# Performance work log

Measured on AMD Instinct MI355X. Metric: run time of the kernel, lower is better.

Reference implementation:

```python
import jax, jax.numpy as jnp
import numpy as np

B, T, D, H, L, K = 64, 512, 256, 256, 2, 3


def setup_inputs() -> dict:
    key = jax.random.key(0)
    ks = jax.random.split(key, 12)
    s = 0.05
    f = jnp.float32
    return {
        "x": jax.random.normal(ks[0], (B, T, D), f),
        # GRUCell params per layer (torch gate order: r, z, n)
        "W_ih": jax.random.normal(ks[1], (L, 3 * H, H), f) * s,
        "b_ih": jax.random.normal(ks[2], (L, 3 * H), f) * s,
        "W_hh": jax.random.normal(ks[3], (L, 3 * H, H), f) * s,
        "b_hh": jax.random.normal(ks[4], (L, 3 * H), f) * s,
        # refinement cell params per layer
        "Wg": jax.random.normal(ks[5], (L, H, 2 * H), f) * s,
        "bg": jax.random.normal(ks[6], (L, H), f) * s,
        "Wt": jax.random.normal(ks[7], (L, H, 2 * H), f) * s,
        "bt": jax.random.normal(ks[8], (L, H), f) * s,
        "Wu": jax.random.normal(ks[9], (L, H, H), f) * s,
        "bu": jax.random.normal(ks[10], (L, H), f) * s,
    }


def reference(x, W_ih, b_ih, W_hh, b_hh, Wg, bg, Wt, bt, Wu, bu):
    def step(hidden, x_t):  # hidden: (L, B, H), x_t: (B, D)
        inp = x_t
        new_hiddens = []
        for l in range(L):
            h = hidden[l]
            # GRU cell (torch semantics)
            gi = inp @ W_ih[l].T + b_ih[l]
            gh = h @ W_hh[l].T + b_hh[l]
            i_r, i_z, i_n = jnp.split(gi, 3, axis=-1)
            h_r, h_z, h_n = jnp.split(gh, 3, axis=-1)
            r = jax.nn.sigmoid(i_r + h_r)
            z = jax.nn.sigmoid(i_z + h_z)
            n = jnp.tanh(i_n + r * h_n)
            h_new = (1.0 - z) * n + z * h
            # recursive refinement
            out = h_new
            rh = h_new
            for _ in range(K):
                comb = jnp.concatenate([out, rh], axis=-1)  # (B, 2H)
                g = jax.nn.sigmoid(comb @ Wg[l].T + bg[l])
                ref = jnp.tanh(comb @ Wt[l].T + bt[l])
                out = g * ref + (1.0 - g) * out
                rh = jnp.tanh(out @ Wu[l].T + bu[l])
            new_hiddens.append(h_new)
            inp = out
        return jnp.stack(new_hiddens, axis=0), inp

    hidden0 = jnp.zeros((L, B, H), x.dtype)
    final_hidden, outs = jax.lax.scan(step, hidden0, jnp.swapaxes(x, 0, 1))
    output = jnp.swapaxes(outs, 0, 1)  # (B, T, H)
    return output, final_hidden
```

## Files before the change

kernel.cpp:

```cpp
#include <hip/hip_runtime.h>

typedef float  f32x4  __attribute__((ext_vector_type(4)));
typedef __bf16 bf16x8 __attribute__((ext_vector_type(8)));

#define NB 64
#define NT 512
#define ND 256
#define NH 256
#define NROW (NB*NT)

#define OFF_WIH 0
#define OFF_WHH 393216
#define OFF_WGT 786432
#define OFF_WU  1310720
#define W_TOTAL 1441792
#define OFF_GI   (W_TOTAL)
#define OFF_OUT0 (OFF_GI + 512*64*768)
#define OFF_OUT1 (OFF_OUT0 + NROW*256)
#define OFF_FLAG (OFF_OUT1 + NROW*256)

#define NW 128

__device__ inline unsigned short f2bu(float f){
  unsigned int u = __builtin_bit_cast(unsigned int, f);
  unsigned int r = u + 0x7fffu + ((u >> 16) & 1u);
  return (unsigned short)(r >> 16);
}
__device__ inline float bf2f(unsigned short u){
  unsigned int v = ((unsigned int)u) << 16;
  return __builtin_bit_cast(float, v);
}
__device__ inline float sigm(float x){ return 1.0f / (1.0f + __expf(-x)); }
__device__ inline float tanhf_(float x){ return 1.0f - 2.0f / (__expf(2.0f * x) + 1.0f); }

#define MFMA(a,b,c) __builtin_amdgcn_mfma_f32_16x16x32_bf16((a),(b),(c),0,0,0)

__device__ inline void gload_lds16(const void* g, void* l){
  __builtin_amdgcn_global_load_lds(
    (const __attribute__((address_space(1))) unsigned int*)g,
    (__attribute__((address_space(3))) unsigned int*)l, 16, 0, 0);
}
__device__ inline bf16x8 ldG(const unsigned short* p){
  return *reinterpret_cast<const bf16x8*>(p);
}
template<int SLP>
__device__ inline void spin_ge(int* p, int tgt){
  while (__hip_atomic_load(p, __ATOMIC_RELAXED, __HIP_MEMORY_SCOPE_AGENT) < tgt)
    __builtin_amdgcn_s_sleep(SLP);
}

__global__ void cvt_weights(const float* __restrict__ Wih, const float* __restrict__ Whh,
                            const float* __restrict__ Wg,  const float* __restrict__ Wt,
                            const float* __restrict__ Wu,  unsigned short* __restrict__ ws){
  int i = blockIdx.x * blockDim.x + threadIdx.x;
  if (i < OFF_WHH) {
    ws[i] = f2bu(Wih[i]);
  } else if (i < OFF_WGT) {
    ws[i] = f2bu(Whh[i - OFF_WHH]);
  } else if (i < OFF_WU) {
    int j = i - OFF_WGT;
    int l = j >> 18; int r = (j >> 9) & 511; int k = j & 511;
    float v = (r < 256) ? Wg[(l * 256 + r) * 512 + k]
                        : Wt[(l * 256 + (r - 256)) * 512 + k];
    ws[i] = f2bu(v);
  } else if (i < W_TOTAL) {
    ws[i] = f2bu(Wu[i - OFF_WU]);
  }
}

__global__ void pack_x(const float* __restrict__ x, unsigned short* __restrict__ xin){
  size_t i = ((size_t)blockIdx.x * blockDim.x + threadIdx.x) * 4;
  float4 v = *reinterpret_cast<const float4*>(x + i);
  ushort4 u; u.x = f2bu(v.x); u.y = f2bu(v.y); u.z = f2bu(v.z); u.w = f2bu(v.w);
  *reinterpret_cast<ushort4*>(xin + i) = u;
}

__global__ __launch_bounds__(1024) void gi_gemm(
    const unsigned short* __restrict__ xin,
    const unsigned short* __restrict__ wih,
    const float* __restrict__ bih, const float* __restrict__ bhh,
    unsigned short* __restrict__ gi)
{
  __shared__ alignas(16) unsigned short sA[64 * 256];
  const int tid = threadIdx.x, blk = blockIdx.x;
  const int ln = tid & 63, wv = tid >> 6, m = ln & 15, lg = ln >> 4;
  {
    const char* src = (const char*)(xin + (size_t)blk * 64 * 256);
    #pragma unroll
    for (int i = 0; i < 2; ++i){
      int o = tid * 16 + i * 16384;
      int r = o >> 9, wb = o & 511;
      gload_lds16(src + (size_t)r * 512 + (wb ^ ((r & 7) << 4)), (char*)sA + o);
    }
  }
  __syncthreads();
  f32x4 acc[3][4] = {};
  #pragma unroll
  for (int kc = 0; kc < 8; ++kc){
    int kk = kc * 32 + lg * 8;
    bf16x8 a[4];
    #pragma unroll
    for (int mt = 0; mt < 4; ++mt){
      int row = mt * 16 + m;
      a[mt] = *(const bf16x8*)((const char*)sA + row * 512 + ((kk * 2) ^ ((row & 7) << 4)));
    }
    #pragma unroll
    for (int g = 0; g < 3; ++g){
      bf16x8 b = ldG(wih + (size_t)(g * 256 + wv * 16 + m) * 256 + kk);
      #pragma unroll
      for (int mt = 0; mt < 4; ++mt) acc[g][mt] = MFMA(a[mt], b, acc[g][mt]);
    }
  }
  const int c = wv * 16 + m;
  #pragma unroll
  for (int g = 0; g < 3; ++g){
    float bias = bih[g * 256 + c] + (g < 2 ? bhh[g * 256 + c] : 0.f);
    #pragma unroll
    for (int mt = 0; mt < 4; ++mt){
      #pragma unroll
      for (int j = 0; j < 4; ++j){
        int row = blk * 64 + mt * 16 + lg * 4 + j;
        int b = row >> 9, t = row & 511;
        gi[((size_t)t * 64 + b) * 768 + g * 256 + c] = f2bu(acc[g][mt][j] + bias);
      }
    }
  }
}

__device__ void chain_role(
    int grp, const unsigned short* __restrict__ gi, const unsigned short* __restrict__ whh,
    const float* __restrict__ bhh, unsigned short* __restrict__ outw,
    float* __restrict__ hfin, int* prog, int* bd, char* smem)
{
  __builtin_amdgcn_s_setprio(1);
  char* hAc = smem;
  const int tid = threadIdx.x;
  const int ln  = tid & 63, wv = tid >> 6;
  const int m   = ln & 15;
  const int lg  = ln >> 4;

  f32x4 wf[3][2][8];
  #pragma unroll
  for (int g = 0; g < 3; ++g)
    #pragma unroll
    for (int s = 0; s < 2; ++s){
      const unsigned short* p = whh + (size_t)(g * 256 + wv * 32 + s * 16 + m) * 256;
      #pragma unroll
      for (int kc = 0; kc < 8; ++kc){
        wf[g][s][kc] = *reinterpret_cast<const f32x4*>(p + kc * 32 + lg * 8);
        asm volatile("" : "+v"(wf[g][s][kc]));
      }
    }

  const int bb   = lg & 1;
  const int su   = lg >> 1;
  const int wcol = wv * 32 + su * 16 + m;
  const int brow = grp * 2 + bb;
  const float bNv = bhh[512 + wcol];

  const int arow  = m & 1;
  const int arows = arow << 4;
  const int rbase = arow * 512;
  const int wbyte = bb * 512 + ((wcol * 2) ^ (bb << 4));

  const unsigned short* gbase = gi + (size_t)brow * 768 + wcol;
  unsigned short* op = outw + (size_t)brow * NT * 256 + wcol;

  if (tid < 256){
    ((unsigned int*)hAc)[tid] = 0;
    ((unsigned int*)(hAc + 1024))[tid] = 0;
  }
  if (bd){
    if (tid == 0){ spin_ge<8>(&bd[0], 16); spin_ge<8>(&bd[1], 16); __threadfence(); }
    __syncthreads();
    (void)__hip_atomic_load(&bd[0], __ATOMIC_ACQUIRE, __HIP_MEMORY_SCOPE_AGENT);
  }
  unsigned int gAr = gbase[0], gAz = gbase[256], gAn = gbase[512];
  unsigned int gBr = gbase[49152], gBz = gbase[49152 + 256], gBn = gbase[49152 + 512];
  float h = 0.f;
  __syncthreads();

  auto body = [&](int t, int curo, unsigned int& GR, unsigned int& GZ, unsigned int& GN){
    float xr = bf2f((unsigned short)GR);
    float xz = bf2f((unsigned short)GZ);
    float xn = bf2f((unsigned short)GN);
    if (t + 2 < NT){
      const unsigned short* gp = gbase + (size_t)(t + 2) * 49152;
      GR = gp[0]; GZ = gp[256]; GN = gp[512];
    }
    f32x4 a00{}, a01{}, a10{}, a11{}, a20{}, a21{};
    #pragma unroll
    for (int kc = 0; kc < 8; ++kc){
      int kb = kc * 64 + lg * 16;
      bf16x8 hv = *(const bf16x8*)(hAc + curo + rbase + (kb ^ arows));
      a00 = MFMA(hv, __builtin_bit_cast(bf16x8, wf[0][0][kc]), a00);
      a01 = MFMA(hv, __builtin_bit_cast(bf16x8, wf[0][1][kc]), a01);
      a10 = MFMA(hv, __builtin_bit_cast(bf16x8, wf[1][0][kc]), a10);
      a11 = MFMA(hv, __builtin_bit_cast(bf16x8, wf[1][1][kc]), a11);
      a20 = MFMA(hv, __builtin_bit_cast(bf16x8, wf[2][0][kc]), a20);
      a21 = MFMA(hv, __builtin_bit_cast(bf16x8, wf[2][1][kc]), a21);
    }
    float aR = su ? (bb ? a01[1] : a01[0]) : (bb ? a00[1] : a00[0]);
    float aZ = su ? (bb ? a11[1] : a11[0]) : (bb ? a10[1] : a10[0]);
    float aN = su ? (bb ? a21[1] : a21[0]) : (bb ? a20[1] : a20[0]);
    float R = sigm(aR + xr);
    float Z = sigm(aZ + xz);
    float N = tanhf_(xn + R * (aN + bNv));
    h = N + Z * (h - N);
    unsigned short hb = f2bu(h);
    *(unsigned short*)(hAc + (curo ^ 1024) + wbyte) = hb;
    op[t * 256] = hb;
    asm volatile("s_waitcnt lgkmcnt(0)" ::: "memory");
    __builtin_amdgcn_sched_barrier(0);
    __builtin_amdgcn_s_barrier();
    __builtin_amdgcn_sched_barrier(0);
  };

  for (int tp = 0; tp < NT; tp += 2){
    if ((tp & 15) == 0){
      if (tp > 0){
        __syncthreads();
        if (tid == 0){
          __threadfence();
          __hip_atomic_store(prog, tp, __ATOMIC_RELEASE, __HIP_MEMORY_SCOPE_AGENT);
        }
      }
      if (bd){
        int B1 = (tp >> 4) + 1;
        if (B1 < 32){
          if (tid == 0){ spin_ge<8>(&bd[B1], 16); __threadfence(); }
          __syncthreads();
          (void)__hip_atomic_load(&bd[B1], __ATOMIC_ACQUIRE, __HIP_MEMORY_SCOPE_AGENT);
        }
      }
    }
    body(tp,     0,    gAr, gAz, gAn);
    body(tp + 1, 1024, gBr, gBz, gBn);
  }
  __syncthreads();
  if (tid == 0){
    __threadfence();
    __hip_atomic_store(prog, NT, __ATOMIC_RELEASE, __HIP_MEMORY_SCOPE_AGENT);
  }
  hfin[(size_t)brow * 256 + wcol] = h;
}

__device__ void worker_role(
    int w, unsigned short* __restrict__ gi,
    const unsigned short* __restrict__ outw0, const unsigned short* __restrict__ outw1,
    const unsigned short* __restrict__ wsb,
    const float* __restrict__ bih, const float* __restrict__ bhh,
    const float* __restrict__ bg, const float* __restrict__ bt, const float* __restrict__ bu,
    float* __restrict__ o, int* flags, char* smem)
{
  const int tid = threadIdx.x;
  const int ln = tid & 63, wv = tid >> 6, m = ln & 15, lg = ln >> 4;

  auto ldA = [&](int row, int kbyte) -> bf16x8 {
    return *(const bf16x8*)(smem + row * 1024 + (kbyte ^ ((row & 7) << 4)));
  };

  for (int i = w; i < 1024; i += NW){
    const int lay = i >> 9, t = i & 511;
    int* prog = &flags[lay * 32];
    if (tid == 0){
      for (int q = 0; q < 32; ++q) spin_ge<32>(&prog[q], t + 1);
      __threadfence();
    }
    __syncthreads();
    (void)__hip_atomic_load(&prog[0], __ATOMIC_ACQUIRE, __HIP_MEMORY_SCOPE_AGENT);

    const unsigned short* src0 = lay ? outw1 : outw0;
    #pragma unroll
    for (int q = 0; q < 8; ++q){
      int ofs = tid * 16 + q * 8192;
      int r = ofs >> 10, wb = ofs & 1023;
      int wb2 = (wb ^ ((r & 7) << 4)) & 511;
      gload_lds16((const char*)(src0 + ((size_t)r * NT + t) * 256) + wb2, smem + ofs);
    }
    __syncthreads();

    const unsigned short* wgt = wsb + OFF_WGT + (size_t)lay * 512 * 512;
    const unsigned short* wu  = wsb + OFF_WU  + (size_t)lay * 256 * 256;
    const float* bgp = bg + lay * 256;
    const float* btp = bt + lay * 256;
    const float* bup = bu + lay * 256;

    for (int iter = 0; iter < 3; ++iter){
      float oo0[4][4], oo1[4][4];
      {
        f32x4 ag[4] = {}, at4[4] = {};
        #pragma unroll 2
        for (int kc = 0; kc < 16; ++kc){
          int kk = kc * 32 + lg * 8;
          bf16x8 Bg = ldG(wgt + (size_t)(      wv * 32 + m) * 512 + kk);
          bf16x8 Bt = ldG(wgt + (size_t)(256 + wv * 32 + m) * 512 + kk);
          #pragma unroll
          for (int mt = 0; mt < 4; ++mt){
            bf16x8 A = ldA(mt * 16 + m, kk * 2);
            ag[mt]  = MFMA(A, Bg, ag[mt]);
            at4[mt] = MFMA(A, Bt, at4[mt]);
          }
        }
        int col = wv * 32 + m;
        float bgv = bgp[col], btv = btp[col];
        #pragma unroll
        for (int mt = 0; mt < 4; ++mt)
          #pragma unroll
          for (int j = 0; j < 4; ++j){
            int row = mt * 16 + lg * 4 + j;
            float old = bf2f(*(unsigned short*)(smem + row * 1024 + ((col * 2) ^ ((row & 7) << 4))));
            float g  = sigm(ag[mt][j] + bgv);
            float rf = tanhf_(at4[mt][j] + btv);
            oo0[mt][j] = g * rf + (1.f - g) * old;
          }
      }
      {
        f32x4 ag[4] = {}, at4[4] = {};
        #pragma unroll 2
        for (int kc = 0; kc < 16; ++kc){
          int kk = kc * 32 + lg * 8;
          bf16x8 Bg = ldG(wgt + (size_t)(      wv * 32 + 16 + m) * 512 + kk);
          bf16x8 Bt = ldG(wgt + (size_t)(256 + wv * 32 + 16 + m) * 512 + kk);
          #pragma unroll
          for (int mt = 0; mt < 4; ++mt){
            bf16x8 A = ldA(mt * 16 + m, kk * 2);
            ag[mt]  = MFMA(A, Bg, ag[mt]);
            at4[mt] = MFMA(A, Bt, at4[mt]);
          }
        }
        int col = wv * 32 + 16 + m;
        float bgv = bgp[col], btv = btp[col];
        #pragma unroll
        for (int mt = 0; mt < 4; ++mt)
          #pragma unroll
          for (int j = 0; j < 4; ++j){
            int row = mt * 16 + lg * 4 + j;
            float old = bf2f(*(unsigned short*)(smem + row * 1024 + ((col * 2) ^ ((row & 7) << 4))));
            float g  = sigm(ag[mt][j] + bgv);
            float rf = tanhf_(at4[mt][j] + btv);
            oo1[mt][j] = g * rf + (1.f - g) * old;
          }
      }
      __syncthreads();
      if (iter == 2 && lay == 1){
        #pragma unroll
        for (int mt = 0; mt < 4; ++mt)
          #pragma unroll
          for (int j = 0; j < 4; ++j){
            int b = mt * 16 + lg * 4 + j;
            o[((size_t)b * NT + t) * 256 + wv * 32 + m]      = oo0[mt][j];
            o[((size_t)b * NT + t) * 256 + wv * 32 + 16 + m] = oo1[mt][j];
          }
      } else {
        #pragma unroll
        for (int mt = 0; mt < 4; ++mt)
          #pragma unroll
          for (int j = 0; j < 4; ++j){
            int row = mt * 16 + lg * 4 + j;
            int c0 = wv * 32 + m, c1 = wv * 32 + 16 + m;
            *(unsigned short*)(smem + row * 1024 + ((c0 * 2) ^ ((row & 7) << 4))) = f2bu(oo0[mt][j]);
            *(unsigned short*)(smem + row * 1024 + ((c1 * 2) ^ ((row & 7) << 4))) = f2bu(oo1[mt][j]);
          }
        __syncthreads();
        if (iter < 2){
          #pragma unroll
          for (int s = 0; s < 2; ++s){
            f32x4 au[4] = {};
            #pragma unroll
            for (int kc = 0; kc < 8; ++kc){
              int kk = kc * 32 + lg * 8;
              bf16x8 Bu = ldG(wu + (size_t)(wv * 32 + s * 16 + m) * 256 + kk);
              #pragma unroll
              for (int mt = 0; mt < 4; ++mt)
                au[mt] = MFMA(ldA(mt * 16 + m, kk * 2), Bu, au[mt]);
            }
            int col = wv * 32 + s * 16 + m;
            float buv = bup[col];
            #pragma unroll
            for (int mt = 0; mt < 4; ++mt)
              #pragma unroll
              for (int j = 0; j < 4; ++j){
                int row = mt * 16 + lg * 4 + j;
                *(unsigned short*)(smem + row * 1024 + (((512 + col * 2)) ^ ((row & 7) << 4)))
                    = f2bu(tanhf_(au[mt][j] + buv));
              }
          }
          __syncthreads();
        }
      }
    }
    if (lay == 0){
      const unsigned short* wih1 = wsb + OFF_WIH + (size_t)768 * 256;
      #pragma unroll
      for (int q = 0; q < 6; ++q){
        int tile = wv + 8 * q;
        int cg = tile * 16 + m;
        f32x4 acc[4] = {};
        #pragma unroll
        for (int kc = 0; kc < 8; ++kc){
          int kk = kc * 32 + lg * 8;
          bf16x8 B = ldG(wih1 + (size_t)cg * 256 + kk);
          #pragma unroll
          for (int mt = 0; mt < 4; ++mt)
            acc[mt] = MFMA(ldA(mt * 16 + m, kk * 2), B, acc[mt]);
        }
        float bias = bih[768 + cg] + (cg < 512 ? bhh[768 + cg] : 0.f);
        #pragma unroll
        for (int mt = 0; mt < 4; ++mt)
          #pragma unroll
          for (int j = 0; j < 4; ++j){
            int b = mt * 16 + lg * 4 + j;
            gi[((size_t)t * 64 + b) * 768 + cg] = f2bu(acc[mt][j] + bias);
          }
      }
      __syncthreads();
      if (tid == 0){
        __threadfence();
        __hip_atomic_fetch_add(&flags[64 + (t >> 4)], 1, __ATOMIC_RELEASE, __HIP_MEMORY_SCOPE_AGENT);
      }
    } else {
      __syncthreads();
    }
  }
}

__global__ __launch_bounds__(512, 2) void mega(
    unsigned short* __restrict__ gi, const unsigned short* __restrict__ wsb,
    const float* __restrict__ bih, const float* __restrict__ bhh,
    const float* __restrict__ bg, const float* __restrict__ bt, const float* __restrict__ bu,
    unsigned short* __restrict__ outw0, unsigned short* __restrict__ outw1,
    float* __restrict__ o, float* __restrict__ hf, int* flags)
{
  extern __shared__ char smem[];
  const int role = blockIdx.x;
  if (role < NW){
    worker_role(role, gi, outw0, outw1, wsb, bih, bhh, bg, bt, bu, o, flags, smem);
  } else if (role < NW + 32){
    chain_role(role - NW, gi, wsb + OFF_WHH, bhh, outw0, hf,
               &flags[role - NW], nullptr, smem);
  } else {
    chain_role(role - NW - 32, gi, wsb + OFF_WHH + 768 * 256, bhh + 768, outw1,
               hf + 64 * 256, &flags[32 + (role - NW - 32)], &flags[64], smem);
  }
}

extern "C" void kernel_launch(void* const* d_in, const int* in_sizes, int n_in,
                              void* d_out, int out_size, void* d_ws, size_t ws_size,
                              hipStream_t stream) {
  const float* x   = (const float*)d_in[0];
  const float* Wih = (const float*)d_in[1];
  const float* bih = (const float*)d_in[2];
  const float* Whh = (const float*)d_in[3];
  const float* bhh = (const float*)d_in[4];
  const float* Wg  = (const float*)d_in[5];
  const float* bg  = (const float*)d_in[6];
  const float* Wt  = (const float*)d_in[7];
  const float* bt  = (const float*)d_in[8];
  const float* Wu  = (const float*)d_in[9];
  const float* bu  = (const float*)d_in[10];
  unsigned short* ws = (unsigned short*)d_ws;
  float* o  = (float*)d_out;
  float* hf = o + (size_t)NB * NT * NH;

  unsigned short* gi    = ws + OFF_GI;
  unsigned short* outw0 = ws + OFF_OUT0;
  unsigned short* outw1 = ws + OFF_OUT1;
  unsigned short* xin   = ws + OFF_OUT1;
  int* flags = (int*)(ws + OFF_FLAG);

  const int MEGA_LDS = 100 * 1024;
  (void)hipFuncSetAttribute((const void*)mega,
                            hipFuncAttributeMaxDynamicSharedMemorySize, MEGA_LDS);

  cvt_weights<<<W_TOTAL / 256, 256, 0, stream>>>(Wih, Whh, Wg, Wt, Wu, ws);
  pack_x<<<(NROW * 256 / 4) / 256, 256, 0, stream>>>(x, xin);
  gi_gemm<<<512, 1024, 0, stream>>>(xin, ws + OFF_WIH, bih, bhh, gi);
  (void)hipMemsetAsync(flags, 0, 96 * sizeof(int), stream);
  mega<<<NW + 64, 512, MEGA_LDS, stream>>>(gi, ws, bih, bhh, bg, bt, bu,
                                           outw0, outw1, o, hf, flags);
}
```

Measured before the change: 1.085 ms.

## Stage GI blocks into LDS in chain role and dynamically schedule layer-1 refinement

The recurrent chain blocks now copy each 16-timestep block of precomputed input-gate values into a double-buffered LDS area with async loads, instead of issuing scattered per-step global loads. Layer-1 refinement tasks are no longer statically assigned to worker blocks; any block that finishes its role, chain blocks included, pulls timesteps from an atomic job counter. The goal is to take global-load latency off the serial recurrence and to use chain blocks for the layer-1 tail work. The cost is more LDS use and counter contention, and chain blocks now exit early into the work queue.

```diff
diff --git a/kernel.cpp b/kernel.cpp
--- a/kernel.cpp
+++ b/kernel.cpp
@@ -76,8 +76,7 @@
 }
 
 __global__ __launch_bounds__(1024) void gi_gemm(
-    const unsigned short* __restrict__ xin,
-    const unsigned short* __restrict__ wih,
+    const unsigned short* __restrict__ xin, const unsigned short* __restrict__ wih,
     const float* __restrict__ bih, const float* __restrict__ bhh,
     unsigned short* __restrict__ gi)
 {
@@ -133,7 +132,8 @@
     float* __restrict__ hfin, int* prog, int* bd, char* smem)
 {
   __builtin_amdgcn_s_setprio(1);
-  char* hAc = smem;
+  char* sGI = smem;
+  char* hAc = smem + 98304;
   const int tid = threadIdx.x;
   const int ln  = tid & 63, wv = tid >> 6;
   const int m   = ln & 15;
@@ -162,32 +162,47 @@
   const int arows = arow << 4;
   const int rbase = arow * 512;
   const int wbyte = bb * 512 + ((wcol * 2) ^ (bb << 4));
-
-  const unsigned short* gbase = gi + (size_t)brow * 768 + wcol;
+  const int goff  = bb * 1536 + wcol * 2;
+
+  const char* gsrc = (const char*)gi + (size_t)(grp * 2) * 1536;
   unsigned short* op = outw + (size_t)brow * NT * 256 + wcol;
 
   if (tid < 256){
     ((unsigned int*)hAc)[tid] = 0;
     ((unsigned int*)(hAc + 1024))[tid] = 0;
   }
-  if (bd){
-    if (tid == 0){ spin_ge<8>(&bd[0], 16); spin_ge<8>(&bd[1], 16); __threadfence(); }
-    __syncthreads();
-    (void)__hip_atomic_load(&bd[0], __ATOMIC_ACQUIRE, __HIP_MEMORY_SCOPE_AGENT);
-  }
-  unsigned int gAr = gbase[0], gAz = gbase[256], gAn = gbase[512];
-  unsigned int gBr = gbase[49152], gBz = gbase[49152 + 256], gBn = gbase[49152 + 512];
+
+  auto bdwait = [&](int B){
+    if (bd && B < 32){
+      if (tid == 0){ spin_ge<8>(&bd[B], 16); __threadfence(); }
+      __syncthreads();
+      (void)__hip_atomic_load(&bd[B], __ATOMIC_ACQUIRE, __HIP_MEMORY_SCOPE_AGENT);
+    }
+  };
+  auto stage = [&](int B){
+    char* dst = sGI + (B & 1) * 49152;
+    const char* src = gsrc + (size_t)B * 16 * 98304;
+    #pragma unroll
+    for (int r = 0; r < 6; ++r){
+      int o = tid * 16 + r * 8192;
+      int tl = o / 3072;
+      int wi = o - tl * 3072;
+      gload_lds16(src + (size_t)tl * 98304 + wi, dst + o);
+    }
+  };
+
+  bdwait(0);
+  stage(0);
+  asm volatile("s_waitcnt vmcnt(0)" ::: "memory");
+  __syncthreads();
+
   float h = 0.f;
-  __syncthreads();
-
-  auto body = [&](int t, int curo, unsigned int& GR, unsigned int& GZ, unsigned int& GN){
-    float xr = bf2f((unsigned short)GR);
-    float xz = bf2f((unsigned short)GZ);
-    float xn = bf2f((unsigned short)GN);
-    if (t + 2 < NT){
-      const unsigned short* gp = gbase + (size_t)(t + 2) * 49152;
-      GR = gp[0]; GZ = gp[256]; GN = gp[512];
-    }
+
+  auto body = [&](int t, int curo){
+    const char* gp = sGI + ((t >> 4) & 1) * 49152 + (t & 15) * 3072 + goff;
+    unsigned short ur = *(const unsigned short*)(gp);
+    unsigned short uz = *(const unsigned short*)(gp + 512);
+    unsigned short un = *(const unsigned short*)(gp + 1024);
     f32x4 a00{}, a01{}, a10{}, a11{}, a20{}, a21{};
     #pragma unroll
     for (int kc = 0; kc < 8; ++kc){
@@ -203,9 +218,9 @@
     float aR = su ? (bb ? a01[1] : a01[0]) : (bb ? a00[1] : a00[0]);
     float aZ = su ? (bb ? a11[1] : a11[0]) : (bb ? a10[1] : a10[0]);
     float aN = su ? (bb ? a21[1] : a21[0]) : (bb ? a20[1] : a20[0]);
-    float R = sigm(aR + xr);
-    float Z = sigm(aZ + xz);
-    float N = tanhf_(xn + R * (aN + bNv));
+    float R = sigm(aR + bf2f(ur));
+    float Z = sigm(aZ + bf2f(uz));
+    float N = tanhf_(bf2f(un) + R * (aN + bNv));
     h = N + Z * (h - N);
     unsigned short hb = f2bu(h);
     *(unsigned short*)(hAc + (curo ^ 1024) + wbyte) = hb;
@@ -216,26 +231,20 @@
     __builtin_amdgcn_sched_barrier(0);
   };
 
-  for (int tp = 0; tp < NT; tp += 2){
-    if ((tp & 15) == 0){
-      if (tp > 0){
-        __syncthreads();
-        if (tid == 0){
-          __threadfence();
-          __hip_atomic_store(prog, tp, __ATOMIC_RELEASE, __HIP_MEMORY_SCOPE_AGENT);
-        }
-      }
-      if (bd){
-        int B1 = (tp >> 4) + 1;
-        if (B1 < 32){
-          if (tid == 0){ spin_ge<8>(&bd[B1], 16); __threadfence(); }
-          __syncthreads();
-          (void)__hip_atomic_load(&bd[B1], __ATOMIC_ACQUIRE, __HIP_MEMORY_SCOPE_AGENT);
-        }
-      }
-    }
-    body(tp,     0,    gAr, gAz, gAn);
-    body(tp + 1, 1024, gBr, gBz, gBn);
+  for (int B = 0; B < 32; ++B){
+    if (B > 0){
+      __syncthreads();
+      if (tid == 0){
+        __threadfence();
+        __hip_atomic_store(prog, 16 * B, __ATOMIC_RELEASE, __HIP_MEMORY_SCOPE_AGENT);
+      }
+    }
+    bdwait(B + 1);
+    if (B + 1 < 32) stage(B + 1);
+    const int t0 = B * 16;
+    #pragma unroll 2
+    for (int tl = 0; tl < 16; ++tl)
+      body(t0 + tl, (tl & 1) ? 1024 : 0);
   }
   __syncthreads();
   if (tid == 0){
@@ -243,11 +252,13 @@
     __hip_atomic_store(prog, NT, __ATOMIC_RELEASE, __HIP_MEMORY_SCOPE_AGENT);
   }
   hfin[(size_t)brow * 256 + wcol] = h;
-}
-
-__device__ void worker_role(
-    int w, unsigned short* __restrict__ gi,
-    const unsigned short* __restrict__ outw0, const unsigned short* __restrict__ outw1,
+  __builtin_amdgcn_s_setprio(0);
+  __syncthreads();
+}
+
+template<int LAY>
+__device__ void refine_task(
+    int t, unsigned short* __restrict__ gi, const unsigned short* __restrict__ src0,
     const unsigned short* __restrict__ wsb,
     const float* __restrict__ bih, const float* __restrict__ bhh,
     const float* __restrict__ bg, const float* __restrict__ bt, const float* __restrict__ bu,
@@ -260,168 +271,130 @@
     return *(const bf16x8*)(smem + row * 1024 + (kbyte ^ ((row & 7) << 4)));
   };
 
-  for (int i = w; i < 1024; i += NW){
-    const int lay = i >> 9, t = i & 511;
-    int* prog = &flags[lay * 32];
-    if (tid == 0){
-      for (int q = 0; q < 32; ++q) spin_ge<32>(&prog[q], t + 1);
-      __threadfence();
-    }
-    __syncthreads();
-    (void)__hip_atomic_load(&prog[0], __ATOMIC_ACQUIRE, __HIP_MEMORY_SCOPE_AGENT);
-
-    const unsigned short* src0 = lay ? outw1 : outw0;
-    #pragma unroll
-    for (int q = 0; q < 8; ++q){
-      int ofs = tid * 16 + q * 8192;
-      int r = ofs >> 10, wb = ofs & 1023;
-      int wb2 = (wb ^ ((r & 7) << 4)) & 511;
-      gload_lds16((const char*)(src0 + ((size_t)r * NT + t) * 256) + wb2, smem + ofs);
-    }
-    __syncthreads();
-
-    const unsigned short* wgt = wsb + OFF_WGT + (size_t)lay * 512 * 512;
-    const unsigned short* wu  = wsb + OFF_WU  + (size_t)lay * 256 * 256;
-    const float* bgp = bg + lay * 256;
-    const float* btp = bt + lay * 256;
-    const float* bup = bu + lay * 256;
-
-    for (int iter = 0; iter < 3; ++iter){
-      float oo0[4][4], oo1[4][4];
-      {
-        f32x4 ag[4] = {}, at4[4] = {};
-        #pragma unroll 2
-        for (int kc = 0; kc < 16; ++kc){
-          int kk = kc * 32 + lg * 8;
-          bf16x8 Bg = ldG(wgt + (size_t)(      wv * 32 + m) * 512 + kk);
-          bf16x8 Bt = ldG(wgt + (size_t)(256 + wv * 32 + m) * 512 + kk);
+  #pragma unroll
+  for (int q = 0; q < 8; ++q){
+    int ofs = tid * 16 + q * 8192;
+    int r = ofs >> 10, wb = ofs & 1023;
+    int wb2 = (wb ^ ((r & 7) << 4)) & 511;
+    gload_lds16((const char*)(src0 + ((size_t)r * NT + t) * 256) + wb2, smem + ofs);
+  }
+  __syncthreads();
+
+  const unsigned short* wgt = wsb + OFF_WGT + (size_t)LAY * 512 * 512;
+  const unsigned short* wu  = wsb + OFF_WU  + (size_t)LAY * 256 * 256;
+  const float* bgp = bg + LAY * 256;
+  const float* btp = bt + LAY * 256;
+  const float* bup = bu + LAY * 256;
+
+  for (int iter = 0; iter < 3; ++iter){
+    float oo0[4][4], oo1[4][4];
+    #pragma unroll
+    for (int s = 0; s < 2; ++s){
+      f32x4 ag[4] = {}, at4[4] = {};
+      #pragma unroll 2
+      for (int kc = 0; kc < 16; ++kc){
+        int kk = kc * 32 + lg * 8;
+        bf16x8 Bg = ldG(wgt + (size_t)(      wv * 32 + s * 16 + m) * 512 + kk);
+        bf16x8 Bt = ldG(wgt + (size_t)(256 + wv * 32 + s * 16 + m) * 512 + kk);
+        #pragma unroll
+        for (int mt = 0; mt < 4; ++mt){
+          bf16x8 A = ldA(mt * 16 + m, kk * 2);
+          ag[mt]  = MFMA(A, Bg, ag[mt]);
+          at4[mt] = MFMA(A, Bt, at4[mt]);
+        }
+      }
+      int col = wv * 32 + s * 16 + m;
+      float bgv = bgp[col], btv = btp[col];
+      #pragma unroll
+      for (int mt = 0; mt < 4; ++mt)
+        #pragma unroll
+        for (int j = 0; j < 4; ++j){
+          int row = mt * 16 + lg * 4 + j;
+          float old = bf2f(*(unsigned short*)(smem + row * 1024 + ((col * 2) ^ ((row & 7) << 4))));
+          float g  = sigm(ag[mt][j] + bgv);
+          float rf = tanhf_(at4[mt][j] + btv);
+          if (s == 0) oo0[mt][j] = g * rf + (1.f - g) * old;
+          else        oo1[mt][j] = g * rf + (1.f - g) * old;
+        }
+    }
+    __syncthreads();
+    if (iter == 2 && LAY == 1){
+      #pragma unroll
+      for (int mt = 0; mt < 4; ++mt)
+        #pragma unroll
+        for (int j = 0; j < 4; ++j){
+          int b = mt * 16 + lg * 4 + j;
+          o[((size_t)b * NT + t) * 256 + wv * 32 + m]      = oo0[mt][j];
+          o[((size_t)b * NT + t) * 256 + wv * 32 + 16 + m] = oo1[mt][j];
+        }
+    } else {
+      #pragma unroll
+      for (int mt = 0; mt < 4; ++mt)
+        #pragma unroll
+        for (int j = 0; j < 4; ++j){
+          int row = mt * 16 + lg * 4 + j;
+          int c0 = wv * 32 + m, c1 = wv * 32 + 16 + m;
+          *(unsigned short*)(smem + row * 1024 + ((c0 * 2) ^ ((row & 7) << 4))) = f2bu(oo0[mt][j]);
+          *(unsigned short*)(smem + row * 1024 + ((c1 * 2) ^ ((row & 7) << 4))) = f2bu(oo1[mt][j]);
+        }
+      __syncthreads();
+      if (iter < 2){
+        #pragma unroll
+        for (int s = 0; s < 2; ++s){
+          f32x4 au[4] = {};
           #pragma unroll
-          for (int mt = 0; mt < 4; ++mt){
-            bf16x8 A = ldA(mt * 16 + m, kk * 2);
-            ag[mt]  = MFMA(A, Bg, ag[mt]);
-            at4[mt] = MFMA(A, Bt, at4[mt]);
-          }
-        }
-        int col = wv * 32 + m;
-        float bgv = bgp[col], btv = btp[col];
-        #pragma unroll
-        for (int mt = 0; mt < 4; ++mt)
-          #pragma unroll
-          for (int j = 0; j < 4; ++j){
-            int row = mt * 16 + lg * 4 + j;
-            float old = bf2f(*(unsigned short*)(smem + row * 1024 + ((col * 2) ^ ((row & 7) << 4))));
-            float g  = sigm(ag[mt][j] + bgv);
-            float rf = tanhf_(at4[mt][j] + btv);
-            oo0[mt][j] = g * rf + (1.f - g) * old;
-          }
-      }
-      {
-        f32x4 ag[4] = {}, at4[4] = {};
-        #pragma unroll 2
-        for (int kc = 0; kc < 16; ++kc){
-          int kk = kc * 32 + lg * 8;
-          bf16x8 Bg = ldG(wgt + (size_t)(      wv * 32 + 16 + m) * 512 + kk);
-          bf16x8 Bt = ldG(wgt + (size_t)(256 + wv * 32 + 16 + m) * 512 + kk);
-          #pragma unroll
-          for (int mt = 0; mt < 4; ++mt){
-            bf16x8 A = ldA(mt * 16 + m, kk * 2);
-            ag[mt]  = MFMA(A, Bg, ag[mt]);
-            at4[mt] = MFMA(A, Bt, at4[mt]);
-          }
-        }
-        int col = wv * 32 + 16 + m;
-        float bgv = bgp[col], btv = btp[col];
-        #pragma unroll
-        for (int mt = 0; mt < 4; ++mt)
-          #pragma unroll
-          for (int j = 0; j < 4; ++j){
-            int row = mt * 16 + lg * 4 + j;
-            float old = bf2f(*(unsigned short*)(smem + row * 1024 + ((col * 2) ^ ((row & 7) << 4))));
-            float g  = sigm(ag[mt][j] + bgv);
-            float rf = tanhf_(at4[mt][j] + btv);
-            oo1[mt][j] = g * rf + (1.f - g) * old;
-          }
-      }
-      __syncthreads();
-      if (iter == 2 && lay == 1){
-        #pragma unroll
-        for (int mt = 0; mt < 4; ++mt)
-          #pragma unroll
-          for (int j = 0; j < 4; ++j){
-            int b = mt * 16 + lg * 4 + j;
-            o[((size_t)b * NT + t) * 256 + wv * 32 + m]      = oo0[mt][j];
-            o[((size_t)b * NT + t) * 256 + wv * 32 + 16 + m] = oo1[mt][j];
-          }
-      } else {
-        #pragma unroll
-        for (int mt = 0; mt < 4; ++mt)
-          #pragma unroll
-          for (int j = 0; j < 4; ++j){
-            int row = mt * 16 + lg * 4 + j;
-            int c0 = wv * 32 + m, c1 = wv * 32 + 16 + m;
-            *(unsigned short*)(smem + row * 1024 + ((c0 * 2) ^ ((row & 7) << 4))) = f2bu(oo0[mt][j]);
-            *(unsigned short*)(smem + row * 1024 + ((c1 * 2) ^ ((row & 7) << 4))) = f2bu(oo1[mt][j]);
-          }
-        __syncthreads();
-        if (iter < 2){
-          #pragma unroll
-          for (int s = 0; s < 2; ++s){
-            f32x4 au[4] = {};
-            #pragma unroll
-            for (int kc = 0; kc < 8; ++kc){
-              int kk = kc * 32 + lg * 8;
-              bf16x8 Bu = ldG(wu + (size_t)(wv * 32 + s * 16 + m) * 256 + kk);
-              #pragma unroll
-              for (int mt = 0; mt < 4; ++mt)
-                au[mt] = MFMA(ldA(mt * 16 + m, kk * 2), Bu, au[mt]);
-            }
-            int col = wv * 32 + s * 16 + m;
-            float buv = bup[col];
+          for (int kc = 0; kc < 8; ++kc){
+            int kk = kc * 32 + lg * 8;
+            bf16x8 Bu = ldG(wu + (size_t)(wv * 32 + s * 16 + m) * 256 + kk);
             #pragma unroll
             for (int mt = 0; mt < 4; ++mt)
-              #pragma unroll
-              for (int j = 0; j < 4; ++j){
-                int row = mt * 16 + lg * 4 + j;
-                *(unsigned short*)(smem + row * 1024 + (((512 + col * 2)) ^ ((row & 7) << 4)))
-                    = f2bu(tanhf_(au[mt][j] + buv));
-              }
+              au[mt] = MFMA(ldA(mt * 16 + m, kk * 2), Bu, au[mt]);
           }
-          __syncthreads();
-        }
-      }
-    }
-    if (lay == 0){
-      const unsigned short* wih1 = wsb + OFF_WIH + (size_t)768 * 256;
-      #pragma unroll
-      for (int q = 0; q < 6; ++q){
-        int tile = wv + 8 * q;
-        int cg = tile * 16 + m;
-        f32x4 acc[4] = {};
-        #pragma unroll
-        for (int kc = 0; kc < 8; ++kc){
-          int kk = kc * 32 + lg * 8;
-          bf16x8 B = ldG(wih1 + (size_t)cg * 256 + kk);
+          int col = wv * 32 + s * 16 + m;
+          float buv = bup[col];
           #pragma unroll
           for (int mt = 0; mt < 4; ++mt)
-            acc[mt] = MFMA(ldA(mt * 16 + m, kk * 2), B, acc[mt]);
-        }
-        float bias = bih[768 + cg] + (cg < 512 ? bhh[768 + cg] : 0.f);
+            #pragma unroll
+            for (int j = 0; j < 4; ++j){
+              int row = mt * 16 + lg * 4 + j;
+              *(unsigned short*)(smem + row * 1024 + (((512 + col * 2)) ^ ((row & 7) << 4)))
+                  = f2bu(tanhf_(au[mt][j] + buv));
+            }
+        }
+        __syncthreads();
+      }
+    }
+  }
+  if (LAY == 0){
+    const unsigned short* wih1 = wsb + OFF_WIH + (size_t)768 * 256;
+    #pragma unroll
+    for (int q = 0; q < 6; ++q){
+      int cg = (wv + 8 * q) * 16 + m;
+      f32x4 acc[4] = {};
+      #pragma unroll
+      for (int kc = 0; kc < 8; ++kc){
+        int kk = kc * 32 + lg * 8;
+        bf16x8 B = ldG(wih1 + (size_t)cg * 256 + kk);
         #pragma unroll
         for (int mt = 0; mt < 4; ++mt)
-          #pragma unroll
-          for (int j = 0; j < 4; ++j){
-            int b = mt * 16 + lg * 4 + j;
-            gi[((size_t)t * 64 + b) * 768 + cg] = f2bu(acc[mt][j] + bias);
-          }
-      }
-      __syncthreads();
-      if (tid == 0){
-        __threadfence();
-        __hip_atomic_fetch_add(&flags[64 + (t >> 4)], 1, __ATOMIC_RELEASE, __HIP_MEMORY_SCOPE_AGENT);
-      }
-    } else {
-      __syncthreads();
-    }
+          acc[mt] = MFMA(ldA(mt * 16 + m, kk * 2), B, acc[mt]);
+      }
+      float bias = bih[768 + cg] + (cg < 512 ? bhh[768 + cg] : 0.f);
+      #pragma unroll
+      for (int mt = 0; mt < 4; ++mt)
+        #pragma unroll
+        for (int j = 0; j < 4; ++j){
+          int b = mt * 16 + lg * 4 + j;
+          gi[((size_t)t * 64 + b) * 768 + cg] = f2bu(acc[mt][j] + bias);
+        }
+    }
+    __syncthreads();
+    if (tid == 0){
+      __threadfence();
+      __hip_atomic_fetch_add(&flags[64 + (t >> 4)], 1, __ATOMIC_RELEASE, __HIP_MEMORY_SCOPE_AGENT);
+    }
+  } else {
+    __syncthreads();
   }
 }
 
@@ -434,14 +407,41 @@
 {
   extern __shared__ char smem[];
   const int role = blockIdx.x;
+  const int tid = threadIdx.x;
+
   if (role < NW){
-    worker_role(role, gi, outw0, outw1, wsb, bih, bhh, bg, bt, bu, o, flags, smem);
+    for (int t = role; t < 512; t += NW){
+      if (tid == 0){
+        for (int q = 0; q < 32; ++q) spin_ge<32>(&flags[q], t + 1);
+        __threadfence();
+      }
+      __syncthreads();
+      (void)__hip_atomic_load(&flags[0], __ATOMIC_ACQUIRE, __HIP_MEMORY_SCOPE_AGENT);
+      refine_task<0>(t, gi, outw0, wsb, bih, bhh, bg, bt, bu, o, flags, smem);
+    }
   } else if (role < NW + 32){
     chain_role(role - NW, gi, wsb + OFF_WHH, bhh, outw0, hf,
                &flags[role - NW], nullptr, smem);
   } else {
     chain_role(role - NW - 32, gi, wsb + OFF_WHH + 768 * 256, bhh + 768, outw1,
                hf + 64 * 256, &flags[32 + (role - NW - 32)], &flags[64], smem);
+  }
+
+  int* jslot = (int*)(smem + 65536);
+  for (;;){
+    if (tid == 0)
+      *jslot = __hip_atomic_fetch_add(&flags[96], 1, __ATOMIC_RELAXED, __HIP_MEMORY_SCOPE_AGENT);
+    __syncthreads();
+    int t = *jslot;
+    __syncthreads();
+    if (t >= 512) break;
+    if (tid == 0){
+      for (int q = 0; q < 32; ++q) spin_ge<32>(&flags[32 + q], t + 1);
+      __threadfence();
+    }
+    __syncthreads();
+    (void)__hip_atomic_load(&flags[32], __ATOMIC_ACQUIRE, __HIP_MEMORY_SCOPE_AGENT);
+    refine_task<1>(t, gi, outw1, wsb, bih, bhh, bg, bt, bu, o, flags, smem);
   }
 }
 
@@ -476,7 +476,7 @@
   cvt_weights<<<W_TOTAL / 256, 256, 0, stream>>>(Wih, Whh, Wg, Wt, Wu, ws);
   pack_x<<<(NROW * 256 / 4) / 256, 256, 0, stream>>>(x, xin);
   gi_gemm<<<512, 1024, 0, stream>>>(xin, ws + OFF_WIH, bih, bhh, gi);
-  (void)hipMemsetAsync(flags, 0, 96 * sizeof(int), stream);
+  (void)hipMemsetAsync(flags, 0, 97 * sizeof(int), stream);
   mega<<<NW + 64, 512, MEGA_LDS, stream>>>(gi, ws, bih, bhh, bg, bt, bu,
                                            outw0, outw1, o, hf, flags);
 }
```

Measured after the change: 1.132 ms. 4.3% more time.
